# Performance work log

Hardware: AMD Instinct MI355X
Metric: run time of the kernel (lower is better)

Reference implementation:

```python
import itertools
import jax, jax.numpy as jnp
import numpy as np

B, S, D = 512, 49, 448
H, KD, RATIO, RES = 8, 32, 4, 7
EKD = KD * RATIO              # expanded key dim = 128
QKV_OUT = H * (2 * KD + EKD)  # 1536
MLP_HID = D * 4               # 1792
EPS = 1e-5
LS_INIT = 1e-5


def _build_bias_idxs():
    points = list(itertools.product(range(RES), range(RES)))
    offsets = {}
    idxs = []
    for p1 in points:
        for p2 in points:
            off = (abs(p1[0] - p2[0]), abs(p1[1] - p2[1]))
            if off not in offsets:
                offsets[off] = len(offsets)
            idxs.append(offsets[off])
    return np.asarray(idxs, dtype=np.int32).reshape(len(points), len(points)), len(offsets)


def setup_inputs() -> dict:
    key = jax.random.key(0)
    ks = jax.random.split(key, 10)
    idxs_np, n_off = _build_bias_idxs()  # (49,49), 49 unique offsets
    std = 0.02
    return {
        "hidden_states": jax.random.normal(ks[0], (B, S, D), jnp.float32),
        "ln1_g": jnp.ones((D,), jnp.float32),
        "ln1_b": jnp.zeros((D,), jnp.float32),
        "qkv_w": jax.random.normal(ks[1], (D, QKV_OUT), jnp.float32) * std,
        "qkv_b": jnp.zeros((QKV_OUT,), jnp.float32),
        "attention_biases": jax.random.normal(ks[2], (H, n_off), jnp.float32) * std,
        "proj_w": jax.random.normal(ks[3], (H * EKD, D), jnp.float32) * std,
        "proj_b": jnp.zeros((D,), jnp.float32),
        "ln2_g": jnp.ones((D,), jnp.float32),
        "ln2_b": jnp.zeros((D,), jnp.float32),
        "mlp_w1": jax.random.normal(ks[4], (D, MLP_HID), jnp.float32) * std,
        "mlp_b1": jnp.zeros((MLP_HID,), jnp.float32),
        "mlp_w2": jax.random.normal(ks[5], (MLP_HID, D), jnp.float32) * std,
        "mlp_b2": jnp.zeros((D,), jnp.float32),
        "ls1": jnp.full((D,), LS_INIT, jnp.float32),
        "ls2": jnp.full((D,), LS_INIT, jnp.float32),
        "attention_bias_idxs": jnp.asarray(idxs_np),
    }


def _layernorm(x, g, b):
    mu = jnp.mean(x, axis=-1, keepdims=True)
    var = jnp.mean(jnp.square(x - mu), axis=-1, keepdims=True)
    return (x - mu) * jax.lax.rsqrt(var + EPS) * g + b


def reference(hidden_states, ln1_g, ln1_b, qkv_w, qkv_b, attention_biases,
              proj_w, proj_b, ln2_g, ln2_b, mlp_w1, mlp_b1, mlp_w2, mlp_b2,
              ls1, ls2, attention_bias_idxs):
    x = hidden_states
    # --- token mixer (self-attention with relative-position bias) ---
    h = _layernorm(x, ln1_g, ln1_b)
    qkv = h @ qkv_w + qkv_b                           # [B,S,1536]
    qkv = qkv.reshape(B, S, H, 2 * KD + EKD)
    q, k, v = jnp.split(qkv, [KD, 2 * KD], axis=3)    # [B,S,H,32/32/128]
    scale = KD ** (-0.5)
    scores = jnp.einsum("bqhd,bkhd->bhqk", q, k) * scale
    bias = attention_biases[:, attention_bias_idxs]   # [H,S,S]
    probs = jax.nn.softmax(scores + bias[None], axis=-1)
    ctx = jnp.einsum("bhqk,bkhd->bqhd", probs, v).reshape(B, S, H * EKD)
    attn_out = ctx @ proj_w + proj_b                  # [B,S,D]
    # --- residual with layerscale (drop_path = identity in eval) ---
    x = x + ls1 * attn_out
    # --- MLP branch ---
    h2 = _layernorm(x, ln2_g, ln2_b)
    m = jax.nn.gelu(h2 @ mlp_w1 + mlp_b1, approximate=False)
    m = m @ mlp_w2 + mlp_b2
    x = x + ls2 * m
    return x
```

## Files before the change

### kernel.cpp

```cpp
#include <hip/hip_runtime.h>
#include <hip/hip_bf16.h>

#define BB 512
#define SS 49
#define DD 448
#define HH 8
#define QKVO 1536
#define MLPH 1792
#define MM (BB*SS)

using bf16_t = __hip_bfloat16;
typedef __attribute__((ext_vector_type(8))) short short8;
typedef __attribute__((ext_vector_type(4))) float f32x4;

__device__ __forceinline__ void gload_lds16(const void* g, void* l) {
  __builtin_amdgcn_global_load_lds(
      (const __attribute__((address_space(1))) void*)g,
      (__attribute__((address_space(3))) void*)l,
      16, 0, 0);
}

__global__ __launch_bounds__(256) void transpose_cast(const float* __restrict__ src,
                                                      bf16_t* __restrict__ dst,
                                                      int R, int C)
{
  __shared__ float tile[32][33];
  const int tx = threadIdx.x & 31, ty = threadIdx.x >> 5;
  const int c0 = blockIdx.x * 32, r0 = blockIdx.y * 32;
#pragma unroll
  for (int i = 0; i < 4; ++i)
    tile[ty + i*8][tx] = src[(size_t)(r0 + ty + i*8) * C + c0 + tx];
  __syncthreads();
#pragma unroll
  for (int i = 0; i < 4; ++i)
    dst[(size_t)(c0 + ty + i*8) * R + r0 + tx] = __float2bfloat16(tile[tx][ty + i*8]);
}

__global__ __launch_bounds__(256) void biasprep_kernel(const float* __restrict__ ab,
                                                       const int* __restrict__ idxs,
                                                       bf16_t* __restrict__ bias_pad)
{
  int idx = blockIdx.x * 256 + threadIdx.x;
  int h = idx >> 12, r = (idx >> 6) & 63, c = idx & 63;
  float v = (r < SS && c < SS) ? ab[h*49 + idxs[r*49 + c]] : -1e30f;
  bias_pad[idx] = __float2bfloat16(v);
}

__global__ __launch_bounds__(256) void ln_kernel(const float* __restrict__ x,
                                                 const float* __restrict__ g,
                                                 const float* __restrict__ b,
                                                 bf16_t* __restrict__ out)
{
  const int w = threadIdx.x >> 6, lane = threadIdx.x & 63;
  const int row = blockIdx.x * 4 + w;
  const float* xr = x + (size_t)row * DD;
  float v[7];
  float s = 0.f;
#pragma unroll
  for (int j = 0; j < 7; ++j) { v[j] = xr[lane + 64*j]; s += v[j]; }
#pragma unroll
  for (int off = 32; off; off >>= 1) s += __shfl_xor(s, off, 64);
  const float mu = s * (1.0f/448.0f);
  float q = 0.f;
#pragma unroll
  for (int j = 0; j < 7; ++j) { float d = v[j] - mu; q += d*d; }
#pragma unroll
  for (int off = 32; off; off >>= 1) q += __shfl_xor(q, off, 64);
  const float rstd = rsqrtf(q * (1.0f/448.0f) + 1e-5f);
  bf16_t* orow = out + (size_t)row * DD;
#pragma unroll
  for (int j = 0; j < 7; ++j) {
    int c = lane + 64*j;
    orow[c] = __float2bfloat16((v[j] - mu) * rstd * g[c] + b[c]);
  }
}

enum { EP_BF16 = 0, EP_RES1 = 1, EP_GELU = 2, EP_RES2 = 3 };

template<int EPI, int BM>
__global__ __launch_bounds__(256, 2) void gemmr_bf16(
    const bf16_t* __restrict__ A, const bf16_t* __restrict__ Bt,
    const float* __restrict__ bias, const float* __restrict__ resid,
    const float* __restrict__ ls, bf16_t* __restrict__ Obf,
    float* __restrict__ Of, int N, int K, int gy)
{
  constexpr int MI = BM / 32;
  constexpr int ABYTES = BM * 128;
  __shared__ __align__(16) char lds[ABYTES + 16384];
  const int t = threadIdx.x;
  const int lane = t & 63;
  const int w = t >> 6;

  const int chunk = gridDim.x >> 3;
  const int lin = blockIdx.x;
  const int swz = (lin & 7) * chunk + (lin >> 3);
  const int m0 = (swz / gy) * BM;
  const int n0 = (swz % gy) * 128;

  const int fr = lane & 15;
  const int fq = lane >> 4;
  const int wm = (w >> 1) * (BM / 2);
  const int wn = (w & 1) * 64;

  f32x4 acc[MI][4];
#pragma unroll
  for (int i = 0; i < MI; ++i)
#pragma unroll
    for (int j = 0; j < 4; ++j)
      acc[i][j] = f32x4{0.f, 0.f, 0.f, 0.f};

  const int rsub = t >> 3;
  const int g8 = (t & 7) ^ (rsub & 7);
  const int wbase = w * 1024;
  const int nkt = K >> 6;

  for (int kt = 0; kt < nkt; ++kt) {
    const int k0 = kt << 6;
#pragma unroll
    for (int i = 0; i < MI; ++i)
      gload_lds16(A + (size_t)(m0 + i*32 + rsub) * K + (k0 + g8*8), lds + i*4096 + wbase);
#pragma unroll
    for (int i = 0; i < 4; ++i) {
      int rb = n0 + i*32 + rsub;
      if (rb >= N) rb = N - 1;
      gload_lds16(Bt + (size_t)rb * K + (k0 + g8*8), lds + ABYTES + i*4096 + wbase);
    }
    __syncthreads();
#pragma unroll
    for (int kk = 0; kk < 2; ++kk) {
      short8 af[MI], bfr[4];
#pragma unroll
      for (int i = 0; i < MI; ++i) {
        const int ra = wm + i*16 + fr;
        const int ca = (fq + kk*4) ^ (ra & 7);
        af[i] = *(const short8*)(lds + ra*128 + ca*16);
      }
#pragma unroll
      for (int i = 0; i < 4; ++i) {
        const int rb2 = wn + i*16 + fr;
        const int cb = (fq + kk*4) ^ (rb2 & 7);
        bfr[i] = *(const short8*)(lds + ABYTES + rb2*128 + cb*16);
      }
#pragma unroll
      for (int mi = 0; mi < MI; ++mi)
#pragma unroll
        for (int ni = 0; ni < 4; ++ni)
          acc[mi][ni] = __builtin_amdgcn_mfma_f32_16x16x32_bf16(af[mi], bfr[ni], acc[mi][ni], 0, 0, 0);
    }
    __syncthreads();
  }

#pragma unroll
  for (int mi = 0; mi < MI; ++mi) {
#pragma unroll
    for (int ni = 0; ni < 4; ++ni) {
      const int col = n0 + wn + ni*16 + fr;
      if (col < N) {
        const float bc = bias[col];
        const int row0 = m0 + wm + mi*16 + fq*4;
#pragma unroll
        for (int ri = 0; ri < 4; ++ri) {
          const size_t o = (size_t)(row0 + ri) * N + col;
          const float v = acc[mi][ni][ri] + bc;
          if constexpr (EPI == EP_BF16) {
            Obf[o] = __float2bfloat16(v);
          } else if constexpr (EPI == EP_GELU) {
            Obf[o] = __float2bfloat16(0.5f * v * (1.0f + erff(v * 0.7071067811865475f)));
          } else if constexpr (EPI == EP_RES1) {
            Of[o] = resid[o] + ls[col] * v;
          } else {
            Of[o] = Of[o] + ls[col] * v;
          }
        }
      }
    }
  }
}

__global__ __launch_bounds__(64) void attn_mfma_kernel(const bf16_t* __restrict__ qkv,
                                                       const bf16_t* __restrict__ bias_pad,
                                                       bf16_t* __restrict__ ctx)
{
  __shared__ __align__(16) bf16_t VsF[64*128];
  __shared__ __align__(16) bf16_t PsF[64*72];
  const int b = blockIdx.x >> 3, h = blockIdx.x & 7;
  const int l = threadIdx.x;
  const int fr = l & 15, g = l >> 4;
  const size_t base = ((size_t)b * SS) * QKVO + (size_t)h * 192;

  for (int c = l; c < 1024; c += 64) {
    const int j = c >> 4, ch = c & 15;
    const int jc = j < SS ? j : SS - 1;
    short8 v = *(const short8*)(qkv + base + (size_t)jc * QKVO + 64 + ch*8);
    *(short8*)(&VsF[j*128 + ((ch ^ (j >> 3)) & 15)*8]) = v;
  }

  short8 qf[4], kf[4];
#pragma unroll
  for (int mi = 0; mi < 4; ++mi) {
    int qr = mi*16 + fr; if (qr > SS-1) qr = SS-1;
    qf[mi] = *(const short8*)(qkv + base + (size_t)qr * QKVO + g*8);
    int kr = mi*16 + fr; if (kr > SS-1) kr = SS-1;
    kf[mi] = *(const short8*)(qkv + base + (size_t)kr * QKVO + 32 + g*8);
  }
  f32x4 sc[4][4];
#pragma unroll
  for (int mi = 0; mi < 4; ++mi)
#pragma unroll
    for (int ni = 0; ni < 4; ++ni)
      sc[mi][ni] = f32x4{0.f,0.f,0.f,0.f};
#pragma unroll
  for (int mi = 0; mi < 4; ++mi)
#pragma unroll
    for (int ni = 0; ni < 4; ++ni)
      sc[mi][ni] = __builtin_amdgcn_mfma_f32_16x16x32_bf16(qf[mi], kf[ni], sc[mi][ni], 0, 0, 0);

  const float scale = 0.17677669529663687f;
  const bf16_t* bp = bias_pad + (size_t)h * 4096;
#pragma unroll
  for (int mi = 0; mi < 4; ++mi) {
#pragma unroll
    for (int ri = 0; ri < 4; ++ri) {
      const int r = mi*16 + g*4 + ri;
      float v0 = sc[mi][0][ri]*scale + __bfloat162float(bp[r*64 +      fr]);
      float v1 = sc[mi][1][ri]*scale + __bfloat162float(bp[r*64 + 16 + fr]);
      float v2 = sc[mi][2][ri]*scale + __bfloat162float(bp[r*64 + 32 + fr]);
      float v3 = sc[mi][3][ri]*scale + __bfloat162float(bp[r*64 + 48 + fr]);
      float m = fmaxf(fmaxf(v0, v1), fmaxf(v2, v3));
#pragma unroll
      for (int off = 8; off; off >>= 1) m = fmaxf(m, __shfl_xor(m, off, 64));
      v0 = __expf(v0 - m); v1 = __expf(v1 - m);
      v2 = __expf(v2 - m); v3 = __expf(v3 - m);
      float s = v0 + v1 + v2 + v3;
#pragma unroll
      for (int off = 8; off; off >>= 1) s += __shfl_xor(s, off, 64);
      const float inv = 1.0f / s;
      PsF[r*72 +      fr] = __float2bfloat16(v0 * inv);
      PsF[r*72 + 16 + fr] = __float2bfloat16(v1 * inv);
      PsF[r*72 + 32 + fr] = __float2bfloat16(v2 * inv);
      PsF[r*72 + 48 + fr] = __float2bfloat16(v3 * inv);
    }
  }
  __syncthreads();

  short8 pf[4][2];
#pragma unroll
  for (int mi = 0; mi < 4; ++mi)
#pragma unroll
    for (int ks = 0; ks < 2; ++ks)
      pf[mi][ks] = *(const short8*)(&PsF[(mi*16 + fr)*72 + ks*32 + g*8]);

#pragma unroll
  for (int ni = 0; ni < 8; ++ni) {
    const int e = ni*16 + fr;
    short8 vf[2];
#pragma unroll
    for (int ks = 0; ks < 2; ++ks) {
      const int jb = ks*32 + g*8;
#pragma unroll
      for (int jj = 0; jj < 8; ++jj) {
        const int j = jb + jj;
        const int ch = ((e >> 3) ^ (j >> 3)) & 15;
        vf[ks][jj] = *(const short*)(&VsF[j*128 + ch*8 + (e & 7)]);
      }
    }
    f32x4 acc2[4];
#pragma unroll
    for (int mi = 0; mi < 4; ++mi) acc2[mi] = f32x4{0.f,0.f,0.f,0.f};
#pragma unroll
    for (int ks = 0; ks < 2; ++ks)
#pragma unroll
      for (int mi = 0; mi < 4; ++mi)
        acc2[mi] = __builtin_amdgcn_mfma_f32_16x16x32_bf16(pf[mi][ks], vf[ks], acc2[mi], 0, 0, 0);
#pragma unroll
    for (int mi = 0; mi < 4; ++mi) {
#pragma unroll
      for (int ri = 0; ri < 4; ++ri) {
        const int q = mi*16 + g*4 + ri;
        if (q < SS)
          ctx[((size_t)b * SS + q) * 1024 + h*128 + e] = __float2bfloat16(acc2[mi][ri]);
      }
    }
  }
}

extern "C" void kernel_launch(void* const* d_in, const int* in_sizes, int n_in,
                              void* d_out, int out_size, void* d_ws, size_t ws_size,
                              hipStream_t stream) {
  const float* x      = (const float*)d_in[0];
  const float* ln1_g  = (const float*)d_in[1];
  const float* ln1_b  = (const float*)d_in[2];
  const float* qkv_w  = (const float*)d_in[3];
  const float* qkv_b  = (const float*)d_in[4];
  const float* ab     = (const float*)d_in[5];
  const float* proj_w = (const float*)d_in[6];
  const float* proj_b = (const float*)d_in[7];
  const float* ln2_g  = (const float*)d_in[8];
  const float* ln2_b  = (const float*)d_in[9];
  const float* w1     = (const float*)d_in[10];
  const float* b1     = (const float*)d_in[11];
  const float* w2     = (const float*)d_in[12];
  const float* b2     = (const float*)d_in[13];
  const float* ls1    = (const float*)d_in[14];
  const float* ls2    = (const float*)d_in[15];
  const int*   idxs   = (const int*)d_in[16];
  float* out = (float*)d_out;
  char* ws = (char*)d_ws;

  bf16_t* h_buf    = (bf16_t*)(ws);
  bf16_t* qkv_buf  = (bf16_t*)(ws + 22478848);
  bf16_t* ctx_buf  = (bf16_t*)(ws + 99549184);
  bf16_t* m_buf    = (bf16_t*)(ws + 22478848);
  bf16_t* qkv_wT   = (bf16_t*)(ws + 150929408);
  bf16_t* proj_wT  = (bf16_t*)(ws + 152305664);
  bf16_t* w1T      = (bf16_t*)(ws + 153223168);
  bf16_t* w2T      = (bf16_t*)(ws + 154828800);
  bf16_t* bias_pad = (bf16_t*)(ws + 156434432);

  transpose_cast<<<dim3(QKVO/32, DD/32),  256, 0, stream>>>(qkv_w,  qkv_wT,  DD,   QKVO);
  transpose_cast<<<dim3(DD/32, 1024/32),  256, 0, stream>>>(proj_w, proj_wT, 1024, DD);
  transpose_cast<<<dim3(MLPH/32, DD/32),  256, 0, stream>>>(w1,     w1T,     DD,   MLPH);
  transpose_cast<<<dim3(DD/32, MLPH/32),  256, 0, stream>>>(w2,     w2T,     MLPH, DD);
  biasprep_kernel<<<128, 256, 0, stream>>>(ab, idxs, bias_pad);

  ln_kernel<<<MM/4, 256, 0, stream>>>(x, ln1_g, ln1_b, h_buf);

  gemmr_bf16<EP_BF16, 128><<<196*12, 256, 0, stream>>>(
      h_buf, qkv_wT, qkv_b, nullptr, nullptr, qkv_buf, nullptr, QKVO, DD, 12);

  attn_mfma_kernel<<<BB*HH, 64, 0, stream>>>(qkv_buf, bias_pad, ctx_buf);

  gemmr_bf16<EP_RES1, 64><<<392*4, 256, 0, stream>>>(
      ctx_buf, proj_wT, proj_b, x, ls1, nullptr, out, DD, 1024, 4);

  ln_kernel<<<MM/4, 256, 0, stream>>>(out, ln2_g, ln2_b, h_buf);

  gemmr_bf16<EP_GELU, 128><<<196*14, 256, 0, stream>>>(
      h_buf, w1T, b1, nullptr, nullptr, m_buf, nullptr, MLPH, DD, 14);

  gemmr_bf16<EP_RES2, 64><<<392*4, 256, 0, stream>>>(
      m_buf, w2T, b2, nullptr, ls2, nullptr, out, DD, MLPH, 4);
}
```

Measured before the change: 324.4 us.

## Double-buffer LDS in bf16 GEMM and use 128-row tiles for all GEMMs

Converts the GEMM kernel to double-buffered dynamic shared memory (64 KB). The next K-tile's global-to-LDS loads are issued while MFMAs run on the current tile, and one barrier per iteration is removed. The BM template is dropped, so the N=448 projection and MLP-down GEMMs now use 128-row tiles with half as many blocks. This trades occupancy and grid size for latency hiding and more reuse per block. The hipFuncSetAttribute calls run on every launch, which adds some host overhead.

```diff
diff --git a/kernel.cpp b/kernel.cpp
--- a/kernel.cpp
+++ b/kernel.cpp
@@ -77,16 +77,14 @@
 
 enum { EP_BF16 = 0, EP_RES1 = 1, EP_GELU = 2, EP_RES2 = 3 };
 
-template<int EPI, int BM>
-__global__ __launch_bounds__(256, 2) void gemmr_bf16(
+template<int EPI>
+__global__ __launch_bounds__(256, 2) void gemmd_bf16(
     const bf16_t* __restrict__ A, const bf16_t* __restrict__ Bt,
     const float* __restrict__ bias, const float* __restrict__ resid,
     const float* __restrict__ ls, bf16_t* __restrict__ Obf,
     float* __restrict__ Of, int N, int K, int gy)
 {
-  constexpr int MI = BM / 32;
-  constexpr int ABYTES = BM * 128;
-  __shared__ __align__(16) char lds[ABYTES + 16384];
+  extern __shared__ __align__(16) char lds[];
   const int t = threadIdx.x;
   const int lane = t & 63;
   const int w = t >> 6;
@@ -94,17 +92,17 @@
   const int chunk = gridDim.x >> 3;
   const int lin = blockIdx.x;
   const int swz = (lin & 7) * chunk + (lin >> 3);
-  const int m0 = (swz / gy) * BM;
+  const int m0 = (swz / gy) * 128;
   const int n0 = (swz % gy) * 128;
 
   const int fr = lane & 15;
   const int fq = lane >> 4;
-  const int wm = (w >> 1) * (BM / 2);
+  const int wm = (w >> 1) * 64;
   const int wn = (w & 1) * 64;
 
-  f32x4 acc[MI][4];
-#pragma unroll
-  for (int i = 0; i < MI; ++i)
+  f32x4 acc[4][4];
+#pragma unroll
+  for (int i = 0; i < 4; ++i)
 #pragma unroll
     for (int j = 0; j < 4; ++j)
       acc[i][j] = f32x4{0.f, 0.f, 0.f, 0.f};
@@ -114,44 +112,59 @@
   const int wbase = w * 1024;
   const int nkt = K >> 6;
 
+  const bf16_t* gA[4];
+  const bf16_t* gB[4];
+#pragma unroll
+  for (int i = 0; i < 4; ++i) {
+    gA[i] = A + (size_t)(m0 + i*32 + rsub) * K + g8*8;
+    int rb = n0 + i*32 + rsub;
+    if (rb >= N) rb = N - 1;
+    gB[i] = Bt + (size_t)rb * K + g8*8;
+  }
+
+#pragma unroll
+  for (int i = 0; i < 4; ++i) {
+    gload_lds16(gA[i], lds + i*4096 + wbase);
+    gload_lds16(gB[i], lds + 16384 + i*4096 + wbase);
+  }
+  __syncthreads();
+
+  int cur = 0;
   for (int kt = 0; kt < nkt; ++kt) {
-    const int k0 = kt << 6;
-#pragma unroll
-    for (int i = 0; i < MI; ++i)
-      gload_lds16(A + (size_t)(m0 + i*32 + rsub) * K + (k0 + g8*8), lds + i*4096 + wbase);
-#pragma unroll
-    for (int i = 0; i < 4; ++i) {
-      int rb = n0 + i*32 + rsub;
-      if (rb >= N) rb = N - 1;
-      gload_lds16(Bt + (size_t)rb * K + (k0 + g8*8), lds + ABYTES + i*4096 + wbase);
-    }
-    __syncthreads();
+    if (kt + 1 < nkt) {
+      char* db = lds + (cur ^ 1) * 32768;
+      const int ko = (kt + 1) << 6;
+#pragma unroll
+      for (int i = 0; i < 4; ++i) {
+        gload_lds16(gA[i] + ko, db + i*4096 + wbase);
+        gload_lds16(gB[i] + ko, db + 16384 + i*4096 + wbase);
+      }
+    }
+    const char* sb = lds + cur * 32768;
 #pragma unroll
     for (int kk = 0; kk < 2; ++kk) {
-      short8 af[MI], bfr[4];
-#pragma unroll
-      for (int i = 0; i < MI; ++i) {
+      short8 af[4], bfr[4];
+#pragma unroll
+      for (int i = 0; i < 4; ++i) {
         const int ra = wm + i*16 + fr;
         const int ca = (fq + kk*4) ^ (ra & 7);
-        af[i] = *(const short8*)(lds + ra*128 + ca*16);
-      }
-#pragma unroll
-      for (int i = 0; i < 4; ++i) {
+        af[i] = *(const short8*)(sb + ra*128 + ca*16);
         const int rb2 = wn + i*16 + fr;
         const int cb = (fq + kk*4) ^ (rb2 & 7);
-        bfr[i] = *(const short8*)(lds + ABYTES + rb2*128 + cb*16);
-      }
-#pragma unroll
-      for (int mi = 0; mi < MI; ++mi)
+        bfr[i] = *(const short8*)(sb + 16384 + rb2*128 + cb*16);
+      }
+#pragma unroll
+      for (int mi = 0; mi < 4; ++mi)
 #pragma unroll
         for (int ni = 0; ni < 4; ++ni)
           acc[mi][ni] = __builtin_amdgcn_mfma_f32_16x16x32_bf16(af[mi], bfr[ni], acc[mi][ni], 0, 0, 0);
     }
     __syncthreads();
-  }
-
-#pragma unroll
-  for (int mi = 0; mi < MI; ++mi) {
+    cur ^= 1;
+  }
+
+#pragma unroll
+  for (int mi = 0; mi < 4; ++mi) {
 #pragma unroll
     for (int ni = 0; ni < 4; ++ni) {
       const int col = n0 + wn + ni*16 + fr;
@@ -317,6 +330,11 @@
   bf16_t* w2T      = (bf16_t*)(ws + 154828800);
   bf16_t* bias_pad = (bf16_t*)(ws + 156434432);
 
+  hipFuncSetAttribute((const void*)&gemmd_bf16<EP_BF16>, hipFuncAttributeMaxDynamicSharedMemorySize, 65536);
+  hipFuncSetAttribute((const void*)&gemmd_bf16<EP_RES1>, hipFuncAttributeMaxDynamicSharedMemorySize, 65536);
+  hipFuncSetAttribute((const void*)&gemmd_bf16<EP_GELU>, hipFuncAttributeMaxDynamicSharedMemorySize, 65536);
+  hipFuncSetAttribute((const void*)&gemmd_bf16<EP_RES2>, hipFuncAttributeMaxDynamicSharedMemorySize, 65536);
+
   transpose_cast<<<dim3(QKVO/32, DD/32),  256, 0, stream>>>(qkv_w,  qkv_wT,  DD,   QKVO);
   transpose_cast<<<dim3(DD/32, 1024/32),  256, 0, stream>>>(proj_w, proj_wT, 1024, DD);
   transpose_cast<<<dim3(MLPH/32, DD/32),  256, 0, stream>>>(w1,     w1T,     DD,   MLPH);
@@ -325,19 +343,19 @@
 
   ln_kernel<<<MM/4, 256, 0, stream>>>(x, ln1_g, ln1_b, h_buf);
 
-  gemmr_bf16<EP_BF16, 128><<<196*12, 256, 0, stream>>>(
+  gemmd_bf16<EP_BF16><<<196*12, 256, 65536, stream>>>(
       h_buf, qkv_wT, qkv_b, nullptr, nullptr, qkv_buf, nullptr, QKVO, DD, 12);
 
   attn_mfma_kernel<<<BB*HH, 64, 0, stream>>>(qkv_buf, bias_pad, ctx_buf);
 
-  gemmr_bf16<EP_RES1, 64><<<392*4, 256, 0, stream>>>(
+  gemmd_bf16<EP_RES1><<<196*4, 256, 65536, stream>>>(
       ctx_buf, proj_wT, proj_b, x, ls1, nullptr, out, DD, 1024, 4);
 
   ln_kernel<<<MM/4, 256, 0, stream>>>(out, ln2_g, ln2_b, h_buf);
 
-  gemmr_bf16<EP_GELU, 128><<<196*14, 256, 0, stream>>>(
+  gemmd_bf16<EP_GELU><<<196*14, 256, 65536, stream>>>(
       h_buf, w1T, b1, nullptr, nullptr, m_buf, nullptr, MLPH, DD, 14);
 
-  gemmr_bf16<EP_RES2, 64><<<392*4, 256, 0, stream>>>(
+  gemmd_bf16<EP_RES2><<<196*4, 256, 65536, stream>>>(
       m_buf, w2T, b2, nullptr, ls2, nullptr, out, DD, MLPH, 4);
 }
```

Measured after the change: 385.4 us. +18.8%, slower.

## Replace GEMM with 256x256-tile, 8-wave, double-buffered pipelined kernel

Applied to the files above, without the earlier changes.

Replaces the single-buffered 128x128/64x128 GEMM with a 512-thread kernel that computes 256x256 output tiles per workgroup. The kernel uses 128KB of dynamic LDS for double buffering, prefetching the next K-slice with async global-to-LDS loads while MFMAs run. It adds explicit barriers, waitcnt control and setprio hints, plus an XCD-aware block remapping. The larger tiles cut grid size sharply (e.g. 196 blocks for the N=448 GEMMs, with wasted columns beyond 448). Together with LDS limits on occupancy, this risks poor CU utilization on the small-N projections.

```diff
diff --git a/kernel.cpp b/kernel.cpp
--- a/kernel.cpp
+++ b/kernel.cpp
@@ -77,87 +77,139 @@
 
 enum { EP_BF16 = 0, EP_RES1 = 1, EP_GELU = 2, EP_RES2 = 3 };
 
-template<int EPI, int BM>
-__global__ __launch_bounds__(256, 2) void gemmr_bf16(
+template<int EPI>
+__global__ __launch_bounds__(512, 2) void gemm8_bf16(
     const bf16_t* __restrict__ A, const bf16_t* __restrict__ Bt,
     const float* __restrict__ bias, const float* __restrict__ resid,
     const float* __restrict__ ls, bf16_t* __restrict__ Obf,
     float* __restrict__ Of, int N, int K, int gy)
 {
-  constexpr int MI = BM / 32;
-  constexpr int ABYTES = BM * 128;
-  __shared__ __align__(16) char lds[ABYTES + 16384];
+  extern __shared__ __align__(16) char lds[];
   const int t = threadIdx.x;
   const int lane = t & 63;
   const int w = t >> 6;
-
-  const int chunk = gridDim.x >> 3;
-  const int lin = blockIdx.x;
-  const int swz = (lin & 7) * chunk + (lin >> 3);
-  const int m0 = (swz / gy) * BM;
-  const int n0 = (swz % gy) * 128;
-
-  const int fr = lane & 15;
-  const int fq = lane >> 4;
-  const int wm = (w >> 1) * (BM / 2);
-  const int wn = (w & 1) * 64;
-
-  f32x4 acc[MI][4];
-#pragma unroll
-  for (int i = 0; i < MI; ++i)
+  const int wm = w >> 2;
+  const int wn = w & 3;
+  const int fr = lane & 15, fq = lane >> 4;
+
+  const int nwg = gridDim.x;
+  const int q8 = nwg >> 3, r8 = nwg & 7;
+  const int xcd = blockIdx.x & 7, bix = blockIdx.x >> 3;
+  const int wg = (xcd < r8 ? xcd*(q8+1) : r8*(q8+1) + (xcd-r8)*q8) + bix;
+  const int m0 = (wg / gy) * 256;
+  const int n0 = (wg % gy) * 256;
+
+  const int NT = K >> 6;
+
+  const int sr0 = t >> 3;
+  const int cge = ((t & 7) ^ (sr0 & 7)) * 8;
+  const bf16_t* gq[4][2];
+#pragma unroll
+  for (int h = 0; h < 2; ++h) {
+    int rb0 = n0 + h*128 + sr0;      if (rb0 >= N) rb0 = N - 1;
+    int rb1 = n0 + h*128 + 64 + sr0; if (rb1 >= N) rb1 = N - 1;
+    gq[h][0]   = Bt + (size_t)rb0 * K + cge;
+    gq[h][1]   = Bt + (size_t)rb1 * K + cge;
+    gq[2+h][0] = A  + (size_t)(m0 + h*128 + sr0) * K + cge;
+    gq[2+h][1] = A  + (size_t)(m0 + h*128 + 64 + sr0) * K + cge;
+  }
+  const int qoff[4] = {32768, 49152, 0, 16384};
+
+#define STAGE_Q(bb, qq, ko) do { \
+    gload_lds16(gq[qq][0] + (ko), lds + (bb)*65536 + qoff[qq] + w*1024); \
+    gload_lds16(gq[qq][1] + (ko), lds + (bb)*65536 + qoff[qq] + 8192 + w*1024); \
+  } while (0)
+
+  const int cx0 = ((fq)     ^ (fr & 7)) * 16;
+  const int cx1 = ((4 + fq) ^ (fr & 7)) * 16;
+  int bo[4];
+#pragma unroll
+  for (int ni = 0; ni < 4; ++ni) {
+    const int rbb = wn*64 + ni*16 + fr;
+    bo[ni] = 32768 + (rbb >> 7)*16384 + (rbb & 127)*128;
+  }
+
+  f32x4 acc[8][4];
+#pragma unroll
+  for (int i = 0; i < 8; ++i)
 #pragma unroll
     for (int j = 0; j < 4; ++j)
       acc[i][j] = f32x4{0.f, 0.f, 0.f, 0.f};
 
-  const int rsub = t >> 3;
-  const int g8 = (t & 7) ^ (rsub & 7);
-  const int wbase = w * 1024;
-  const int nkt = K >> 6;
-
-  for (int kt = 0; kt < nkt; ++kt) {
-    const int k0 = kt << 6;
-#pragma unroll
-    for (int i = 0; i < MI; ++i)
-      gload_lds16(A + (size_t)(m0 + i*32 + rsub) * K + (k0 + g8*8), lds + i*4096 + wbase);
-#pragma unroll
-    for (int i = 0; i < 4; ++i) {
-      int rb = n0 + i*32 + rsub;
-      if (rb >= N) rb = N - 1;
-      gload_lds16(Bt + (size_t)rb * K + (k0 + g8*8), lds + ABYTES + i*4096 + wbase);
-    }
-    __syncthreads();
-#pragma unroll
-    for (int kk = 0; kk < 2; ++kk) {
-      short8 af[MI], bfr[4];
-#pragma unroll
-      for (int i = 0; i < MI; ++i) {
-        const int ra = wm + i*16 + fr;
-        const int ca = (fq + kk*4) ^ (ra & 7);
-        af[i] = *(const short8*)(lds + ra*128 + ca*16);
-      }
-#pragma unroll
-      for (int i = 0; i < 4; ++i) {
-        const int rb2 = wn + i*16 + fr;
-        const int cb = (fq + kk*4) ^ (rb2 & 7);
-        bfr[i] = *(const short8*)(lds + ABYTES + rb2*128 + cb*16);
-      }
-#pragma unroll
-      for (int mi = 0; mi < MI; ++mi)
-#pragma unroll
-        for (int ni = 0; ni < 4; ++ni)
-          acc[mi][ni] = __builtin_amdgcn_mfma_f32_16x16x32_bf16(af[mi], bfr[ni], acc[mi][ni], 0, 0, 0);
-    }
-    __syncthreads();
-  }
-
-#pragma unroll
-  for (int mi = 0; mi < MI; ++mi) {
+  STAGE_Q(0, 0, 0); STAGE_Q(0, 1, 0); STAGE_Q(0, 2, 0); STAGE_Q(0, 3, 0);
+  STAGE_Q(1, 0, 64); STAGE_Q(1, 1, 64);
+  asm volatile("s_waitcnt vmcnt(4)" ::: "memory");
+  __builtin_amdgcn_sched_barrier(0);
+  __builtin_amdgcn_s_barrier();
+  __builtin_amdgcn_sched_barrier(0);
+
+  for (int T = 0; T < NT; ++T) {
+    const int b = T & 1;
+    const char* base = lds + b * 65536;
+    short8 bfr[4][2];
+#pragma unroll
+    for (int q2 = 0; q2 < 4; ++q2) {
+      short8 af[2][2];
+#pragma unroll
+      for (int j = 0; j < 2; ++j) {
+        const int ro = wm*16384 + ((q2*2 + j)*16 + fr)*128;
+        af[j][0] = *(const short8*)(base + ro + cx0);
+        af[j][1] = *(const short8*)(base + ro + cx1);
+      }
+      if (q2 == 0) {
+#pragma unroll
+        for (int ni = 0; ni < 4; ++ni) {
+          bfr[ni][0] = *(const short8*)(base + bo[ni] + cx0);
+          bfr[ni][1] = *(const short8*)(base + bo[ni] + cx1);
+        }
+      }
+      if (q2 == 1 && T + 1 < NT) {
+        const int ko = (T + 1) * 64;
+        STAGE_Q(b ^ 1, 2, ko);
+        STAGE_Q(b ^ 1, 3, ko);
+      }
+      __builtin_amdgcn_sched_barrier(0);
+      __builtin_amdgcn_s_barrier();
+      asm volatile("s_waitcnt lgkmcnt(0)" ::: "memory");
+      __builtin_amdgcn_sched_barrier(0);
+      __builtin_amdgcn_s_setprio(1);
+#pragma unroll
+      for (int ks = 0; ks < 2; ++ks)
+#pragma unroll
+        for (int j = 0; j < 2; ++j)
+#pragma unroll
+          for (int ni = 0; ni < 4; ++ni)
+            acc[q2*2 + j][ni] = __builtin_amdgcn_mfma_f32_16x16x32_bf16(
+                af[j][ks], bfr[ni][ks], acc[q2*2 + j][ni], 0, 0, 0);
+      __builtin_amdgcn_s_setprio(0);
+      __builtin_amdgcn_sched_barrier(0);
+      __builtin_amdgcn_s_barrier();
+      __builtin_amdgcn_sched_barrier(0);
+    }
+    if (T + 1 < NT) {
+      if (T + 2 < NT) {
+        const int ko2 = (T + 2) * 64;
+        STAGE_Q(b, 0, ko2);
+        STAGE_Q(b, 1, ko2);
+        asm volatile("s_waitcnt vmcnt(4)" ::: "memory");
+      } else {
+        asm volatile("s_waitcnt vmcnt(0)" ::: "memory");
+      }
+      __builtin_amdgcn_sched_barrier(0);
+      __builtin_amdgcn_s_barrier();
+      __builtin_amdgcn_sched_barrier(0);
+    }
+  }
+#undef STAGE_Q
+
+#pragma unroll
+  for (int mi = 0; mi < 8; ++mi) {
 #pragma unroll
     for (int ni = 0; ni < 4; ++ni) {
-      const int col = n0 + wn + ni*16 + fr;
+      const int col = n0 + wn*64 + ni*16 + fr;
       if (col < N) {
         const float bc = bias[col];
-        const int row0 = m0 + wm + mi*16 + fq*4;
+        const int row0 = m0 + wm*128 + mi*16 + fq*4;
 #pragma unroll
         for (int ri = 0; ri < 4; ++ri) {
           const size_t o = (size_t)(row0 + ri) * N + col;
@@ -317,6 +369,11 @@
   bf16_t* w2T      = (bf16_t*)(ws + 154828800);
   bf16_t* bias_pad = (bf16_t*)(ws + 156434432);
 
+  hipFuncSetAttribute((const void*)&gemm8_bf16<EP_BF16>, hipFuncAttributeMaxDynamicSharedMemorySize, 131072);
+  hipFuncSetAttribute((const void*)&gemm8_bf16<EP_RES1>, hipFuncAttributeMaxDynamicSharedMemorySize, 131072);
+  hipFuncSetAttribute((const void*)&gemm8_bf16<EP_GELU>, hipFuncAttributeMaxDynamicSharedMemorySize, 131072);
+  hipFuncSetAttribute((const void*)&gemm8_bf16<EP_RES2>, hipFuncAttributeMaxDynamicSharedMemorySize, 131072);
+
   transpose_cast<<<dim3(QKVO/32, DD/32),  256, 0, stream>>>(qkv_w,  qkv_wT,  DD,   QKVO);
   transpose_cast<<<dim3(DD/32, 1024/32),  256, 0, stream>>>(proj_w, proj_wT, 1024, DD);
   transpose_cast<<<dim3(MLPH/32, DD/32),  256, 0, stream>>>(w1,     w1T,     DD,   MLPH);
@@ -325,19 +382,19 @@
 
   ln_kernel<<<MM/4, 256, 0, stream>>>(x, ln1_g, ln1_b, h_buf);
 
-  gemmr_bf16<EP_BF16, 128><<<196*12, 256, 0, stream>>>(
-      h_buf, qkv_wT, qkv_b, nullptr, nullptr, qkv_buf, nullptr, QKVO, DD, 12);
+  gemm8_bf16<EP_BF16><<<98*6, 512, 131072, stream>>>(
+      h_buf, qkv_wT, qkv_b, nullptr, nullptr, qkv_buf, nullptr, QKVO, DD, 6);
 
   attn_mfma_kernel<<<BB*HH, 64, 0, stream>>>(qkv_buf, bias_pad, ctx_buf);
 
-  gemmr_bf16<EP_RES1, 64><<<392*4, 256, 0, stream>>>(
-      ctx_buf, proj_wT, proj_b, x, ls1, nullptr, out, DD, 1024, 4);
+  gemm8_bf16<EP_RES1><<<98*2, 512, 131072, stream>>>(
+      ctx_buf, proj_wT, proj_b, x, ls1, nullptr, out, DD, 1024, 2);
 
   ln_kernel<<<MM/4, 256, 0, stream>>>(out, ln2_g, ln2_b, h_buf);
 
-  gemmr_bf16<EP_GELU, 128><<<196*14, 256, 0, stream>>>(
-      h_buf, w1T, b1, nullptr, nullptr, m_buf, nullptr, MLPH, DD, 14);
-
-  gemmr_bf16<EP_RES2, 64><<<392*4, 256, 0, stream>>>(
-      m_buf, w2T, b2, nullptr, ls2, nullptr, out, DD, MLPH, 4);
-}
+  gemm8_bf16<EP_GELU><<<98*7, 512, 131072, stream>>>(
+      h_buf, w1T, b1, nullptr, nullptr, m_buf, nullptr, MLPH, DD, 7);
+
+  gemm8_bf16<EP_RES2><<<98*2, 512, 131072, stream>>>(
+      m_buf, w2T, b2, nullptr, ls2, nullptr, out, DD, MLPH, 2);
+}
```

Measured after the change: 394.3 us. +21.5%, slower.
